# Kernel optimization log

Measured on AMD Instinct MI355X. Metric: run time of the kernel, lower is better.

Reference implementation:

```python
import jax, jax.numpy as jnp
import numpy as np

D_MODEL = 1024
N_HEADS = 16
ADAPTIVE_TEMP = 1.0
LN_EPS = 1e-5


def _sinusoidal_pe(max_len, d_model):
    pos = np.arange(max_len)[:, None].astype(np.float32)
    div = np.exp(np.arange(0, d_model, 2).astype(np.float32) * (-np.log(10000.0) / d_model))
    pe = np.zeros((max_len, d_model), dtype=np.float32)
    pe[:, 0::2] = np.sin(pos * div)
    pe[:, 1::2] = np.cos(pos * div)
    return jnp.asarray(pe)


def _mlp2(q, w1, b1, w2, b2):
    # Linear(1,h) -> ReLU -> Linear(h,d)
    return jax.nn.relu(q @ w1 + b1) @ w2 + b2


def setup_inputs() -> dict:
    key = jax.random.key(0)
    ks = jax.random.split(key, 24)
    B, T, D = 2, 2048, D_MODEL
    H2 = D // 2
    s = 0.02
    inp = {
        "x": jax.random.normal(ks[0], (B, T, D), jnp.float32),
        "quantile": jax.random.uniform(ks[1], (B, 1), jnp.float32),
        "quantile_importance": jax.random.uniform(ks[2], (100,), jnp.float32),
        "Wq": jax.random.normal(ks[3], (D, D), jnp.float32) * s,
        "bq": jnp.zeros((D,), jnp.float32),
        "Wk": jax.random.normal(ks[4], (D, D), jnp.float32) * s,
        "bk": jnp.zeros((D,), jnp.float32),
        "Wv": jax.random.normal(ks[5], (D, D), jnp.float32) * s,
        "bv": jnp.zeros((D,), jnp.float32),
        "Wo": jax.random.normal(ks[6], (D, D), jnp.float32) * s,
        "bo": jnp.zeros((D,), jnp.float32),
        "qpq_w1": jax.random.normal(ks[7], (1, H2), jnp.float32) * s,
        "qpq_b1": jnp.zeros((H2,), jnp.float32),
        "qpq_w2": jax.random.normal(ks[8], (H2, D), jnp.float32) * s,
        "qpq_b2": jnp.zeros((D,), jnp.float32),
        "qpk_w1": jax.random.normal(ks[9], (1, H2), jnp.float32) * s,
        "qpk_b1": jnp.zeros((H2,), jnp.float32),
        "qpk_w2": jax.random.normal(ks[10], (H2, D), jnp.float32) * s,
        "qpk_b2": jnp.zeros((D,), jnp.float32),
        "qpv_w1": jax.random.normal(ks[11], (1, H2), jnp.float32) * s,
        "qpv_b1": jnp.zeros((H2,), jnp.float32),
        "qpv_w2": jax.random.normal(ks[12], (H2, D), jnp.float32) * s,
        "qpv_b2": jnp.zeros((D,), jnp.float32),
        "ln_g": jnp.ones((D,), jnp.float32),
        "ln_b": jnp.zeros((D,), jnp.float32),
    }
    return inp


def reference(x, quantile, quantile_importance,
              Wq, bq, Wk, bk, Wv, bv, Wo, bo,
              qpq_w1, qpq_b1, qpq_w2, qpq_b2,
              qpk_w1, qpk_b1, qpk_w2, qpk_b2,
              qpv_w1, qpv_b1, qpv_w2, qpv_b2,
              ln_g, ln_b):
    B, T, D = x.shape
    H = N_HEADS
    dk = D // H

    # positional encoding
    x = x + _sinusoidal_pe(T, D)

    # quantile-conditioned embeddings [B, D]
    q_embed = _mlp2(quantile, qpq_w1, qpq_b1, qpq_w2, qpq_b2)
    k_embed = _mlp2(quantile, qpk_w1, qpk_b1, qpk_w2, qpk_b2)
    v_embed = _mlp2(quantile, qpv_w1, qpv_b1, qpv_w2, qpv_b2)

    # importance weight per batch (no-grad buffer lookup)
    buf = jax.lax.stop_gradient(quantile_importance)
    idx = jnp.clip((quantile[:, 0] * 100).astype(jnp.int32), 0, 99)
    mx = buf.max()
    imp = buf[idx]
    imp = jnp.where(mx > 0, imp / mx, imp)  # [B]

    Q = (x @ Wq + bq) + q_embed[:, None, :]
    K = (x @ Wk + bk) + k_embed[:, None, :]
    V = (x @ Wv + bv) + v_embed[:, None, :]

    # [B, H, T, dk]
    Q = Q.reshape(B, T, H, dk).transpose(0, 2, 1, 3)
    K = K.reshape(B, T, H, dk).transpose(0, 2, 1, 3)
    V = V.reshape(B, T, H, dk).transpose(0, 2, 1, 3)

    scores = jnp.einsum('bhtd,bhsd->bhts', Q, K) / jnp.sqrt(jnp.float32(dk))
    scale = 1.0 + imp * ADAPTIVE_TEMP  # [B]
    scores = scores * scale[:, None, None, None]

    attn = jax.nn.softmax(scores, axis=-1)  # dropout is identity at inference
    out = jnp.einsum('bhts,bhsd->bhtd', attn, V)
    out = out.transpose(0, 2, 1, 3).reshape(B, T, D)
    out = out @ Wo + bo

    y = x + out
    mu = y.mean(axis=-1, keepdims=True)
    var = y.var(axis=-1, keepdims=True)
    return (y - mu) / jnp.sqrt(var + LN_EPS) * ln_g + ln_b
```

## Files before the change

### kernel.cpp

```cpp
#include <hip/hip_runtime.h>

#define D 1024
#define T 2048
#define BATCH 2
#define NR 4096
#define NH 16
#define HID 512

typedef unsigned short u16;
typedef unsigned int u32;
typedef unsigned long long u64;
typedef float f32x4 __attribute__((ext_vector_type(4)));
typedef float f32x16 __attribute__((ext_vector_type(16)));
typedef __bf16 bf16x8 __attribute__((ext_vector_type(8)));

__device__ __forceinline__ u16 f2bf(float f) {
    union { __bf16 h; u16 u; } c; c.h = (__bf16)f; return c.u;
}

__device__ __forceinline__ u32 cvtpk(float a, float b) {
    u32 r;
    asm("v_cvt_pk_bf16_f32 %0, %1, %2" : "=v"(r) : "v"(a), "v"(b));
    return r;
}

__device__ __forceinline__ void plswap(u32& x, u32& y) {
    asm volatile("v_permlane32_swap_b32 %0, %1" : "+v"(x), "+v"(y));
}

__device__ __forceinline__ float fmax3(float a, float b, float c) {
    float r; asm("v_max3_f32 %0, %1, %2, %3" : "=v"(r) : "v"(a), "v"(b), "v"(c)); return r;
}

__device__ __forceinline__ float vmax16(const f32x16& v) {
    float c0 = fmax3(v[0], v[1], v[2]);
    float c1 = fmax3(v[3], v[4], v[5]);
    float c2 = fmax3(v[6], v[7], v[8]);
    float c3 = fmax3(v[9], v[10], v[11]);
    c0 = fmax3(c0, v[12], v[13]);
    c1 = fmax3(c1, v[14], v[15]);
    c0 = fmax3(c0, c1, c2);
    return fmaxf(c0, c3);
}

__device__ __forceinline__ void gload16(const u16* g, u16* l) {
    __builtin_amdgcn_global_load_lds(
        (const __attribute__((address_space(1))) unsigned int*)g,
        (__attribute__((address_space(3))) unsigned int*)l,
        16, 0, 0);
}

__device__ __forceinline__ int swz8(int row) {
    return (row & 7) ^ ((row >> 3) & 3);
}

__global__ __launch_bounds__(256) void k_mlp1(const float* __restrict__ qtl,
        const float* __restrict__ w1q, const float* __restrict__ b1q, const float* __restrict__ w2q,
        const float* __restrict__ w1k, const float* __restrict__ b1k, const float* __restrict__ w2k,
        const float* __restrict__ w1v, const float* __restrict__ b1v, const float* __restrict__ w2v,
        const float* __restrict__ qimp, float* __restrict__ part, float* __restrict__ scl)
{
    int dc = blockIdx.x;
    int jc = blockIdx.y;
    int wb = blockIdx.z;
    int which = wb >> 1, b = wb & 1;
    const float *w1, *b1, *w2;
    if (which == 0)      { w1 = w1q; b1 = b1q; w2 = w2q; }
    else if (which == 1) { w1 = w1k; b1 = b1k; w2 = w2k; }
    else                 { w1 = w1v; b1 = b1v; w2 = w2v; }
    int tid = threadIdx.x;
    __shared__ float h[128];
    if (tid < 128) {
        int j = jc * 128 + tid;
        h[tid] = fmaxf(qtl[b] * w1[j] + b1[j], 0.0f);
    }
    __syncthreads();
    int d = dc * 256 + tid;
    float acc = 0.0f;
    for (int j = 0; j < 128; ++j) acc += h[j] * w2[(size_t)(jc * 128 + j) * D + d];
    part[((size_t)wb * 4 + jc) * D + d] = acc;
    if (dc == 0 && jc == 0 && wb == 0 && tid < BATCH) {
        float mx = qimp[0];
        for (int i = 1; i < 100; ++i) mx = fmaxf(mx, qimp[i]);
        float q = qtl[tid];
        int idx = (int)(q * 100.0f);
        idx = idx < 0 ? 0 : (idx > 99 ? 99 : idx);
        float imp = qimp[idx];
        if (mx > 0.0f) imp /= mx;
        scl[tid] = 1.0f + imp;
    }
}

__global__ __launch_bounds__(256) void k_mlp2(const float* __restrict__ part,
        const float* __restrict__ b2q, const float* __restrict__ b2k, const float* __restrict__ b2v,
        float* __restrict__ embeds)
{
    int dc = blockIdx.x;
    int wb = blockIdx.y;
    int which = wb >> 1;
    const float* b2 = which == 0 ? b2q : which == 1 ? b2k : b2v;
    int d = dc * 256 + threadIdx.x;
    float acc = b2[d];
    #pragma unroll
    for (int jc = 0; jc < 4; ++jc) acc += part[((size_t)wb * 4 + jc) * D + d];
    embeds[(size_t)wb * D + d] = acc;
}

__global__ __launch_bounds__(256) void k_prep(const float* __restrict__ x,
                                              float* __restrict__ xpe, u16* __restrict__ xpeb,
                                              const float* __restrict__ Wq, const float* __restrict__ Wk,
                                              const float* __restrict__ Wv, const float* __restrict__ Wo,
                                              u16* __restrict__ Wt)
{
    if (blockIdx.x < 4096) {
        int idx = (blockIdx.x * 256 + threadIdx.x) * 4;
        int d = idx & (D - 1);
        int t = (idx >> 10) & (T - 1);
        const float KL = -0.0089944731946f;
        float ft = (float)t;
        float dv0 = __expf((float)d * KL);
        float dv1 = __expf((float)(d + 2) * KL);
        float a0 = ft * dv0, a1 = ft * dv1;
        float4 xv = *reinterpret_cast<const float4*>(x + idx);
        float4 r;
        r.x = xv.x + __sinf(a0);
        r.y = xv.y + __cosf(a0);
        r.z = xv.z + __sinf(a1);
        r.w = xv.w + __cosf(a1);
        *reinterpret_cast<float4*>(xpe + idx) = r;
        ushort4 o;
        o.x = f2bf(r.x); o.y = f2bf(r.y); o.z = f2bf(r.z); o.w = f2bf(r.w);
        *reinterpret_cast<ushort4*>(xpeb + idx) = o;
        return;
    }
    __shared__ float tile[64][65];
    int bi = blockIdx.x - 4096;
    int z = bi >> 8;
    const float* W = z == 0 ? Wq : z == 1 ? Wk : z == 2 ? Wv : Wo;
    u16* out = Wt + (size_t)z * D * D;
    int n0 = (bi & 15) * 64, k0 = ((bi >> 4) & 15) * 64;
    int r = threadIdx.x >> 4;
    int c4 = (threadIdx.x & 15) * 4;
    #pragma unroll
    for (int rr = 0; rr < 64; rr += 16) {
        float4 v = *reinterpret_cast<const float4*>(W + (size_t)(k0 + r + rr) * D + n0 + c4);
        tile[r + rr][c4 + 0] = v.x; tile[r + rr][c4 + 1] = v.y;
        tile[r + rr][c4 + 2] = v.z; tile[r + rr][c4 + 3] = v.w;
    }
    __syncthreads();
    #pragma unroll
    for (int rr = 0; rr < 64; rr += 16) {
        ushort4 o;
        o.x = f2bf(tile[c4 + 0][r + rr]);
        o.y = f2bf(tile[c4 + 1][r + rr]);
        o.z = f2bf(tile[c4 + 2][r + rr]);
        o.w = f2bf(tile[c4 + 3][r + rr]);
        *reinterpret_cast<ushort4*>(out + (size_t)(n0 + r + rr) * D + k0 + c4) = o;
    }
}

__device__ __forceinline__ void gemm128(const u16* __restrict__ Ag, const u16* __restrict__ Bg,
                                        int m0, int n0, f32x16 acc[2][2])
{
    __shared__ u16 As[128 * 64];
    __shared__ u16 Bs[128 * 64];
    const int tid = threadIdx.x;
    const int lane = tid & 63, wave = tid >> 6;
    const int wr = wave >> 1, wc = wave & 1;
    const int l31 = lane & 31, hb = lane >> 5;
    #pragma unroll
    for (int mi = 0; mi < 2; ++mi)
        #pragma unroll
        for (int ni = 0; ni < 2; ++ni)
            #pragma unroll
            for (int e = 0; e < 16; ++e) acc[mi][ni][e] = 0.0f;

    for (int kt = 0; kt < 16; ++kt) {
        __syncthreads();
        #pragma unroll
        for (int c = 0; c < 4; ++c) {
            int ci = c * 256 + tid;
            int row = ci >> 3;
            int sl = (ci & 7) ^ swz8(row);
            gload16(Ag + (size_t)(m0 + row) * D + kt * 64 + sl * 8, As + (size_t)ci * 8);
            gload16(Bg + (size_t)(n0 + row) * D + kt * 64 + sl * 8, Bs + (size_t)ci * 8);
        }
        __syncthreads();
        #pragma unroll
        for (int ks = 0; ks < 4; ++ks) {
            bf16x8 af[2], bfr[2];
            #pragma unroll
            for (int mi = 0; mi < 2; ++mi) {
                int ra = wr * 64 + mi * 32 + l31;
                int sa = (2 * ks + hb) ^ swz8(ra);
                af[mi] = *reinterpret_cast<const bf16x8*>((const char*)As + ra * 128 + sa * 16);
                int rb = wc * 64 + mi * 32 + l31;
                int sb = (2 * ks + hb) ^ swz8(rb);
                bfr[mi] = *reinterpret_cast<const bf16x8*>((const char*)Bs + rb * 128 + sb * 16);
            }
            #pragma unroll
            for (int mi = 0; mi < 2; ++mi)
                #pragma unroll
                for (int ni = 0; ni < 2; ++ni)
                    acc[mi][ni] = __builtin_amdgcn_mfma_f32_32x32x16_bf16(af[mi], bfr[ni], acc[mi][ni], 0, 0, 0);
        }
    }
}

__global__ __launch_bounds__(256, 2)
void k_qkv(const u16* __restrict__ A, const u16* __restrict__ Wt,
           const float* __restrict__ bq, const float* __restrict__ bk, const float* __restrict__ bv,
           const float* __restrict__ embeds, const float* __restrict__ scl,
           u16* __restrict__ Qo, u16* __restrict__ Ko, u16* __restrict__ Vt)
{
    int which = blockIdx.z;
    const u16* Bg = Wt + (size_t)which * D * D;
    const float* bias = which == 0 ? bq : which == 1 ? bk : bv;
    const float* emb = embeds + which * (BATCH * D);
    int m0 = blockIdx.x * 128, n0 = blockIdx.y * 128;
    f32x16 acc[2][2];
    gemm128(A, Bg, m0, n0, acc);
    int lane = threadIdx.x & 63, wave = threadIdx.x >> 6;
    int wr = wave >> 1, wc = wave & 1;
    int l31 = lane & 31, hb = lane >> 5;
    if (which < 2) {
        u16* Out = which == 0 ? Qo : Ko;
        float sc0 = 1.0f, sc1 = 1.0f;
        if (which == 0) {
            sc0 = scl[0] * 0.125f * 1.44269504f;
            sc1 = scl[1] * 0.125f * 1.44269504f;
        }
        #pragma unroll
        for (int ni = 0; ni < 2; ++ni) {
            int c = n0 + wc * 64 + ni * 32 + l31;
            float add0 = bias[c] + emb[c];
            float add1 = bias[c] + emb[D + c];
            #pragma unroll
            for (int mi = 0; mi < 2; ++mi) {
                #pragma unroll
                for (int reg = 0; reg < 16; ++reg) {
                    int r = m0 + wr * 64 + mi * 32 + (reg & 3) + 8 * (reg >> 2) + 4 * hb;
                    float v = (r >> 11) ? (acc[mi][ni][reg] + add1) * sc1
                                        : (acc[mi][ni][reg] + add0) * sc0;
                    Out[(size_t)r * D + c] = f2bf(v);
                }
            }
        }
    } else {
        #pragma unroll
        for (int ni = 0; ni < 2; ++ni) {
            int c = n0 + wc * 64 + ni * 32 + l31;
            int hh = c >> 6, cc = c & 63;
            float add0 = bias[c] + emb[c];
            float add1 = bias[c] + emb[D + c];
            #pragma unroll
            for (int mi = 0; mi < 2; ++mi) {
                #pragma unroll
                for (int g2 = 0; g2 < 4; ++g2) {
                    int r = m0 + wr * 64 + mi * 32 + 8 * g2 + 4 * hb;
                    int bb = r >> 11;
                    int t = r & (T - 1);
                    float add = bb ? add1 : add0;
                    ushort4 o;
                    o.x = f2bf(acc[mi][ni][4 * g2 + 0] + add);
                    o.y = f2bf(acc[mi][ni][4 * g2 + 1] + add);
                    o.z = f2bf(acc[mi][ni][4 * g2 + 2] + add);
                    o.w = f2bf(acc[mi][ni][4 * g2 + 3] + add);
                    *reinterpret_cast<ushort4*>(Vt + ((size_t)((bb * NH + hh) * 64 + cc)) * T + t) = o;
                }
            }
        }
    }
}

__global__ __launch_bounds__(512, 4)
void k_attn(const u16* __restrict__ Q, const u16* __restrict__ K, const u16* __restrict__ Vt,
            u16* __restrict__ AO)
{
    __shared__ u16 Ks[2][2][64 * 64];
    __shared__ u16 Vs[2][2][64 * 64];
    int bh = blockIdx.x;
    int b = bh >> 4, hh = bh & 15;
    int q0 = blockIdx.y * 128;
    int tid = threadIdx.x;
    int lane = tid & 63, w = tid >> 6;
    int half = w >> 2, wq = w & 3;
    int q31 = lane & 31, h = lane >> 5;
    int sh = tid >> 8, sti = tid & 255;
    int kvb = sh * 1024;

    bf16x8 qf[4];
    {
        const u16* qp = Q + (size_t)(b * T + q0 + wq * 32 + q31) * D + hh * 64 + h * 8;
        #pragma unroll
        for (int ds = 0; ds < 4; ++ds)
            qf[ds] = *reinterpret_cast<const bf16x8*>(qp + ds * 16);
    }

    f32x16 o0, o1;
    #pragma unroll
    for (int e = 0; e < 16; ++e) { o0[e] = 0.0f; o1[e] = 0.0f; }
    float m_run = -1e30f, l_run = 0.0f;

    #pragma unroll
    for (int c = 0; c < 2; ++c) {
        int ci = c * 256 + sti;
        int row = ci >> 3;
        int sl = (ci & 7) ^ swz8(row);
        gload16(K + (size_t)(b * T + kvb + row) * D + hh * 64 + sl * 8, Ks[sh][0] + (size_t)ci * 8);
        gload16(Vt + (size_t)(bh * 64 + row) * T + kvb + sl * 8, Vs[sh][0] + (size_t)ci * 8);
    }
    __syncthreads();

    for (int kt = 0; kt < 16; ++kt) {
        int cur = kt & 1;
        if (kt < 15) {
            int t0 = kvb + (kt + 1) * 64;
            #pragma unroll
            for (int c = 0; c < 2; ++c) {
                int ci = c * 256 + sti;
                int row = ci >> 3;
                int sl = (ci & 7) ^ swz8(row);
                gload16(K + (size_t)(b * T + t0 + row) * D + hh * 64 + sl * 8, Ks[sh][cur ^ 1] + (size_t)ci * 8);
                gload16(Vt + (size_t)(bh * 64 + row) * T + t0 + sl * 8, Vs[sh][cur ^ 1] + (size_t)ci * 8);
            }
        }
        const char* Ksc = (const char*)Ks[half][cur];
        const char* Vsc = (const char*)Vs[half][cur];

        f32x16 s[2];
        #pragma unroll
        for (int k2 = 0; k2 < 2; ++k2)
            #pragma unroll
            for (int e = 0; e < 16; ++e) s[k2][e] = 0.0f;
        __builtin_amdgcn_s_setprio(1);
        #pragma unroll
        for (int k2 = 0; k2 < 2; ++k2) {
            int rk = k2 * 32 + q31;
            int xm = swz8(rk);
            #pragma unroll
            for (int ds = 0; ds < 4; ++ds) {
                int sp = (2 * ds + h) ^ xm;
                bf16x8 kf = *reinterpret_cast<const bf16x8*>(Ksc + rk * 128 + sp * 16);
                s[k2] = __builtin_amdgcn_mfma_f32_32x32x16_bf16(kf, qf[ds], s[k2], 0, 0, 0);
            }
        }
        __builtin_amdgcn_s_setprio(0);

        float mt = fmaxf(vmax16(s[0]), vmax16(s[1]));
        mt = fmaxf(mt, __shfl_xor(mt, 32, 64));
        bool skip = __all((int)(mt <= m_run + 11.0f));
        if (!skip) {
            float mn = fmaxf(m_run, mt);
            float corr = __builtin_exp2f(m_run - mn);
            m_run = mn;
            l_run *= corr;
            #pragma unroll
            for (int reg = 0; reg < 16; ++reg) {
                int src = ((reg & 3) + 8 * (reg >> 2)) + ((lane & 32) >> 3);
                float cr = __shfl(corr, src, 64);
                o0[reg] *= cr;
                o1[reg] *= cr;
            }
        }
        float ps0 = 0.0f, ps1 = 0.0f, ps2 = 0.0f, ps3 = 0.0f;
        #pragma unroll
        for (int k2 = 0; k2 < 2; ++k2)
            #pragma unroll
            for (int e = 0; e < 16; ++e) {
                float p = __builtin_exp2f(s[k2][e] - m_run);
                s[k2][e] = p;
                if ((e & 3) == 0) ps0 += p; else if ((e & 3) == 1) ps1 += p;
                else if ((e & 3) == 2) ps2 += p; else ps3 += p;
            }
        float psum = (ps0 + ps1) + (ps2 + ps3);
        psum += __shfl_xor(psum, 32, 64);
        l_run += psum;

        __builtin_amdgcn_s_setprio(1);
        #pragma unroll
        for (int k2 = 0; k2 < 2; ++k2) {
            u32 w0 = cvtpk(s[k2][0], s[k2][1]),   w1 = cvtpk(s[k2][2], s[k2][3]);
            u32 w2 = cvtpk(s[k2][4], s[k2][5]),   w3 = cvtpk(s[k2][6], s[k2][7]);
            u32 w4 = cvtpk(s[k2][8], s[k2][9]),   w5 = cvtpk(s[k2][10], s[k2][11]);
            u32 w6 = cvtpk(s[k2][12], s[k2][13]), w7 = cvtpk(s[k2][14], s[k2][15]);
            plswap(w0, w2); plswap(w1, w3);
            plswap(w4, w6); plswap(w5, w7);
            union { bf16x8 v; u32 u[4]; } plo, phi;
            plo.u[0] = w0; plo.u[1] = w1; plo.u[2] = w2; plo.u[3] = w3;
            phi.u[0] = w4; phi.u[1] = w5; phi.u[2] = w6; phi.u[3] = w7;
            int rv0 = q31, rv1 = 32 + q31;
            int x0 = swz8(rv0), x1 = swz8(rv1);
            int klo = 2 * k2, khi = 2 * k2 + 1;
            bf16x8 vf;
            vf = *reinterpret_cast<const bf16x8*>(Vsc + rv0 * 128 + (((2 * klo + h) ^ x0) << 4));
            o0 = __builtin_amdgcn_mfma_f32_32x32x16_bf16(plo.v, vf, o0, 0, 0, 0);
            vf = *reinterpret_cast<const bf16x8*>(Vsc + rv1 * 128 + (((2 * klo + h) ^ x1) << 4));
            o1 = __builtin_amdgcn_mfma_f32_32x32x16_bf16(plo.v, vf, o1, 0, 0, 0);
            vf = *reinterpret_cast<const bf16x8*>(Vsc + rv0 * 128 + (((2 * khi + h) ^ x0) << 4));
            o0 = __builtin_amdgcn_mfma_f32_32x32x16_bf16(phi.v, vf, o0, 0, 0, 0);
            vf = *reinterpret_cast<const bf16x8*>(Vsc + rv1 * 128 + (((2 * khi + h) ^ x1) << 4));
            o1 = __builtin_amdgcn_mfma_f32_32x32x16_bf16(phi.v, vf, o1, 0, 0, 0);
        }
        __builtin_amdgcn_s_setprio(0);
        __syncthreads();
    }

    float* ML = (float*)Ks;
    float* OB = (float*)Vs;
    if (half == 1) {
        if (h == 0) {
            ML[(wq * 2 + 0) * 32 + q31] = m_run;
            ML[(wq * 2 + 1) * 32 + q31] = l_run;
        }
        #pragma unroll
        for (int reg = 0; reg < 16; ++reg) {
            int row = (reg & 3) + 8 * (reg >> 2) + 4 * h;
            OB[((size_t)wq * 32 + row) * 64 + q31] = o0[reg];
            OB[((size_t)wq * 32 + row) * 64 + 32 + q31] = o1[reg];
        }
    }
    __syncthreads();
    if (half == 0) {
        float mB = ML[(wq * 2 + 0) * 32 + q31];
        float lB = ML[(wq * 2 + 1) * 32 + q31];
        float mn = fmaxf(m_run, mB);
        float ca = __builtin_exp2f(m_run - mn);
        float cb = __builtin_exp2f(mB - mn);
        float lf = ca * l_run + cb * lB;
        float fa = ca / lf, fb = cb / lf;
        #pragma unroll
        for (int reg = 0; reg < 16; ++reg) {
            int src = ((reg & 3) + 8 * (reg >> 2)) + ((lane & 32) >> 3);
            float far = __shfl(fa, src, 64);
            float fbr = __shfl(fb, src, 64);
            int row = (reg & 3) + 8 * (reg >> 2) + 4 * h;
            float b0 = OB[((size_t)wq * 32 + row) * 64 + q31];
            float b1 = OB[((size_t)wq * 32 + row) * 64 + 32 + q31];
            int qr = q0 + wq * 32 + row;
            size_t off = (size_t)(b * T + qr) * D + hh * 64 + q31;
            AO[off] = f2bf(o0[reg] * far + b0 * fbr);
            AO[off + 32] = f2bf(o1[reg] * far + b1 * fbr);
        }
    }
}

__global__ __launch_bounds__(256, 2)
void k_ogemm(const u16* __restrict__ A, const u16* __restrict__ Wt,
             const float* __restrict__ bo, const float* __restrict__ xpe,
             float* __restrict__ y)
{
    int m0 = blockIdx.x * 128, n0 = blockIdx.y * 128;
    f32x16 acc[2][2];
    gemm128(A, Wt, m0, n0, acc);
    int lane = threadIdx.x & 63, wave = threadIdx.x >> 6;
    int wr = wave >> 1, wc = wave & 1;
    int l31 = lane & 31, hb = lane >> 5;
    #pragma unroll
    for (int ni = 0; ni < 2; ++ni) {
        int c = n0 + wc * 64 + ni * 32 + l31;
        float bc = bo[c];
        #pragma unroll
        for (int mi = 0; mi < 2; ++mi) {
            #pragma unroll
            for (int reg = 0; reg < 16; ++reg) {
                int r = m0 + wr * 64 + mi * 32 + (reg & 3) + 8 * (reg >> 2) + 4 * hb;
                y[(size_t)r * D + c] = acc[mi][ni][reg] + bc + xpe[(size_t)r * D + c];
            }
        }
    }
}

__global__ __launch_bounds__(256) void k_ln(const float* __restrict__ y, const float* __restrict__ g,
                                            const float* __restrict__ bb, float* __restrict__ out)
{
    int row = blockIdx.x;
    int tid = threadIdx.x;
    const float* yr = y + (size_t)row * D;
    float4 v = *reinterpret_cast<const float4*>(yr + tid * 4);
    float s = v.x + v.y + v.z + v.w;
    float s2 = v.x * v.x + v.y * v.y + v.z * v.z + v.w * v.w;
    #pragma unroll
    for (int off = 1; off < 64; off <<= 1) {
        s += __shfl_xor(s, off, 64);
        s2 += __shfl_xor(s2, off, 64);
    }
    __shared__ float red[8];
    int wave = tid >> 6, lane = tid & 63;
    if (lane == 0) { red[wave] = s; red[4 + wave] = s2; }
    __syncthreads();
    s = red[0] + red[1] + red[2] + red[3];
    s2 = red[4] + red[5] + red[6] + red[7];
    float mu = s * (1.0f / 1024.0f);
    float var = s2 * (1.0f / 1024.0f) - mu * mu;
    float rstd = rsqrtf(var + 1e-5f);
    float4 gv = *reinterpret_cast<const float4*>(g + tid * 4);
    float4 bv = *reinterpret_cast<const float4*>(bb + tid * 4);
    float4 o;
    o.x = (v.x - mu) * rstd * gv.x + bv.x;
    o.y = (v.y - mu) * rstd * gv.y + bv.y;
    o.z = (v.z - mu) * rstd * gv.z + bv.z;
    o.w = (v.w - mu) * rstd * gv.w + bv.w;
    *reinterpret_cast<float4*>(out + (size_t)row * D + tid * 4) = o;
}

extern "C" void kernel_launch(void* const* d_in, const int* in_sizes, int n_in,
                              void* d_out, int out_size, void* d_ws, size_t ws_size,
                              hipStream_t stream)
{
    const float* x    = (const float*)d_in[0];
    const float* qtl  = (const float*)d_in[1];
    const float* qimp = (const float*)d_in[2];
    const float* Wq = (const float*)d_in[3];
    const float* bq = (const float*)d_in[4];
    const float* Wk = (const float*)d_in[5];
    const float* bk = (const float*)d_in[6];
    const float* Wv = (const float*)d_in[7];
    const float* bv = (const float*)d_in[8];
    const float* Wo = (const float*)d_in[9];
    const float* bo = (const float*)d_in[10];
    const float* qpq_w1 = (const float*)d_in[11];
    const float* qpq_b1 = (const float*)d_in[12];
    const float* qpq_w2 = (const float*)d_in[13];
    const float* qpq_b2 = (const float*)d_in[14];
    const float* qpk_w1 = (const float*)d_in[15];
    const float* qpk_b1 = (const float*)d_in[16];
    const float* qpk_w2 = (const float*)d_in[17];
    const float* qpk_b2 = (const float*)d_in[18];
    const float* qpv_w1 = (const float*)d_in[19];
    const float* qpv_b1 = (const float*)d_in[20];
    const float* qpv_w2 = (const float*)d_in[21];
    const float* qpv_b2 = (const float*)d_in[22];
    const float* ln_g = (const float*)d_in[23];
    const float* ln_b = (const float*)d_in[24];
    (void)in_sizes; (void)n_in; (void)out_size; (void)ws_size;

    char* w = (char*)d_ws;
    float* xpe   = (float*)(w);
    u16* xpeb    = (u16*)(w + (16u << 20));
    u16* Wt      = (u16*)(w + (24u << 20));
    u16* Qb      = (u16*)(w + (32u << 20));
    u16* Kb      = (u16*)(w + (40u << 20));
    u16* Vtb     = (u16*)(w + (48u << 20));
    u16* AOb     = (u16*)(w + (56u << 20));
    float* yb    = (float*)(w + (32u << 20));
    float* emb   = (float*)(w + (64u << 20));
    float* scl   = (float*)(w + (64u << 20) + 32768);
    float* part  = (float*)(w + (64u << 20) + 65536);

    k_mlp1<<<dim3(4, 4, 6), 256, 0, stream>>>(qtl,
        qpq_w1, qpq_b1, qpq_w2,
        qpk_w1, qpk_b1, qpk_w2,
        qpv_w1, qpv_b1, qpv_w2,
        qimp, part, scl);
    k_mlp2<<<dim3(4, 6), 256, 0, stream>>>(part, qpq_b2, qpk_b2, qpv_b2, emb);
    k_prep<<<5120, 256, 0, stream>>>(x, xpe, xpeb, Wq, Wk, Wv, Wo, Wt);
    k_qkv<<<dim3(32, 8, 3), 256, 0, stream>>>(xpeb, Wt, bq, bk, bv, emb, scl, Qb, Kb, Vtb);
    k_attn<<<dim3(32, 16), 512, 0, stream>>>(Qb, Kb, Vtb, AOb);
    k_ogemm<<<dim3(32, 8), 256, 0, stream>>>(AOb, Wt + (size_t)3 * D * D, bo, xpe, yb);
    k_ln<<<4096, 256, 0, stream>>>(yb, ln_g, ln_b, (float*)d_out);
}
```

Measured before the change: 149.0 us.

## Fold MLP embedding kernels into prep and store residual/pre-LN in bf16

Merges the two small quantile-MLP kernels into extra blocks of the prep kernel, removing two launches and the partial-sum buffer. It also drops the fp32 copy of x+PE, with the output GEMM reading the bf16 copy for the residual, and stores the pre-LayerNorm tensor in bf16 rather than fp32. This cuts global memory traffic in prep, ogemm and layernorm at the cost of extra bf16 rounding in the residual and LN input. The 24 MLP blocks now loop over all 512 hidden units serially, which may leave them as a tail on the prep kernel.

Measured after the change: 150.4 us. About the same (+0.9%).

```diff
diff --git a/kernel.cpp b/kernel.cpp
--- a/kernel.cpp
+++ b/kernel.cpp
@@ -16,6 +16,9 @@
 
 __device__ __forceinline__ u16 f2bf(float f) {
     union { __bf16 h; u16 u; } c; c.h = (__bf16)f; return c.u;
+}
+__device__ __forceinline__ float bf2f(u16 u) {
+    union { u32 u; float f; } c; c.u = ((u32)u) << 16; return c.f;
 }
 
 __device__ __forceinline__ u32 cvtpk(float a, float b) {
@@ -54,32 +57,78 @@
     return (row & 7) ^ ((row >> 3) & 3);
 }
 
-__global__ __launch_bounds__(256) void k_mlp1(const float* __restrict__ qtl,
-        const float* __restrict__ w1q, const float* __restrict__ b1q, const float* __restrict__ w2q,
-        const float* __restrict__ w1k, const float* __restrict__ b1k, const float* __restrict__ w2k,
-        const float* __restrict__ w1v, const float* __restrict__ b1v, const float* __restrict__ w2v,
-        const float* __restrict__ qimp, float* __restrict__ part, float* __restrict__ scl)
-{
-    int dc = blockIdx.x;
-    int jc = blockIdx.y;
-    int wb = blockIdx.z;
+__global__ __launch_bounds__(256) void k_prep(const float* __restrict__ x, u16* __restrict__ xpeb,
+        const float* __restrict__ Wq, const float* __restrict__ Wk,
+        const float* __restrict__ Wv, const float* __restrict__ Wo, u16* __restrict__ Wt,
+        const float* __restrict__ qtl, const float* __restrict__ qimp,
+        const float* __restrict__ w1q, const float* __restrict__ b1q, const float* __restrict__ w2q, const float* __restrict__ b2q,
+        const float* __restrict__ w1k, const float* __restrict__ b1k, const float* __restrict__ w2k, const float* __restrict__ b2k,
+        const float* __restrict__ w1v, const float* __restrict__ b1v, const float* __restrict__ w2v, const float* __restrict__ b2v,
+        float* __restrict__ embeds, float* __restrict__ scl)
+{
+    int tid = threadIdx.x;
+    if (blockIdx.x < 4096) {
+        int idx = (blockIdx.x * 256 + tid) * 4;
+        int d = idx & (D - 1);
+        int t = (idx >> 10) & (T - 1);
+        const float KL = -0.0089944731946f;
+        float ft = (float)t;
+        float dv0 = __expf((float)d * KL);
+        float dv1 = __expf((float)(d + 2) * KL);
+        float a0 = ft * dv0, a1 = ft * dv1;
+        float4 xv = *reinterpret_cast<const float4*>(x + idx);
+        ushort4 o;
+        o.x = f2bf(xv.x + __sinf(a0));
+        o.y = f2bf(xv.y + __cosf(a0));
+        o.z = f2bf(xv.z + __sinf(a1));
+        o.w = f2bf(xv.w + __cosf(a1));
+        *reinterpret_cast<ushort4*>(xpeb + idx) = o;
+        return;
+    }
+    if (blockIdx.x < 5120) {
+        __shared__ float tile[64][65];
+        int bi = blockIdx.x - 4096;
+        int z = bi >> 8;
+        const float* W = z == 0 ? Wq : z == 1 ? Wk : z == 2 ? Wv : Wo;
+        u16* out = Wt + (size_t)z * D * D;
+        int n0 = (bi & 15) * 64, k0 = ((bi >> 4) & 15) * 64;
+        int r = tid >> 4;
+        int c4 = (tid & 15) * 4;
+        #pragma unroll
+        for (int rr = 0; rr < 64; rr += 16) {
+            float4 v = *reinterpret_cast<const float4*>(W + (size_t)(k0 + r + rr) * D + n0 + c4);
+            tile[r + rr][c4 + 0] = v.x; tile[r + rr][c4 + 1] = v.y;
+            tile[r + rr][c4 + 2] = v.z; tile[r + rr][c4 + 3] = v.w;
+        }
+        __syncthreads();
+        #pragma unroll
+        for (int rr = 0; rr < 64; rr += 16) {
+            ushort4 o;
+            o.x = f2bf(tile[c4 + 0][r + rr]);
+            o.y = f2bf(tile[c4 + 1][r + rr]);
+            o.z = f2bf(tile[c4 + 2][r + rr]);
+            o.w = f2bf(tile[c4 + 3][r + rr]);
+            *reinterpret_cast<ushort4*>(out + (size_t)(n0 + r + rr) * D + k0 + c4) = o;
+        }
+        return;
+    }
+    __shared__ float h[HID];
+    int bi2 = blockIdx.x - 5120;
+    int dc = bi2 & 3, wb = bi2 >> 2;
     int which = wb >> 1, b = wb & 1;
-    const float *w1, *b1, *w2;
-    if (which == 0)      { w1 = w1q; b1 = b1q; w2 = w2q; }
-    else if (which == 1) { w1 = w1k; b1 = b1k; w2 = w2k; }
-    else                 { w1 = w1v; b1 = b1v; w2 = w2v; }
-    int tid = threadIdx.x;
-    __shared__ float h[128];
-    if (tid < 128) {
-        int j = jc * 128 + tid;
-        h[tid] = fmaxf(qtl[b] * w1[j] + b1[j], 0.0f);
-    }
+    const float *w1, *b1, *w2, *b2;
+    if (which == 0)      { w1 = w1q; b1 = b1q; w2 = w2q; b2 = b2q; }
+    else if (which == 1) { w1 = w1k; b1 = b1k; w2 = w2k; b2 = b2k; }
+    else                 { w1 = w1v; b1 = b1v; w2 = w2v; b2 = b2v; }
+    float qv = qtl[b];
+    h[tid] = fmaxf(qv * w1[tid] + b1[tid], 0.0f);
+    h[tid + 256] = fmaxf(qv * w1[tid + 256] + b1[tid + 256], 0.0f);
     __syncthreads();
     int d = dc * 256 + tid;
-    float acc = 0.0f;
-    for (int j = 0; j < 128; ++j) acc += h[j] * w2[(size_t)(jc * 128 + j) * D + d];
-    part[((size_t)wb * 4 + jc) * D + d] = acc;
-    if (dc == 0 && jc == 0 && wb == 0 && tid < BATCH) {
+    float acc = b2[d];
+    for (int j = 0; j < HID; ++j) acc += h[j] * w2[(size_t)j * D + d];
+    embeds[(size_t)wb * D + d] = acc;
+    if (bi2 == 0 && tid < BATCH) {
         float mx = qimp[0];
         for (int i = 1; i < 100; ++i) mx = fmaxf(mx, qimp[i]);
         float q = qtl[tid];
@@ -88,74 +137,6 @@
         float imp = qimp[idx];
         if (mx > 0.0f) imp /= mx;
         scl[tid] = 1.0f + imp;
-    }
-}
-
-__global__ __launch_bounds__(256) void k_mlp2(const float* __restrict__ part,
-        const float* __restrict__ b2q, const float* __restrict__ b2k, const float* __restrict__ b2v,
-        float* __restrict__ embeds)
-{
-    int dc = blockIdx.x;
-    int wb = blockIdx.y;
-    int which = wb >> 1;
-    const float* b2 = which == 0 ? b2q : which == 1 ? b2k : b2v;
-    int d = dc * 256 + threadIdx.x;
-    float acc = b2[d];
-    #pragma unroll
-    for (int jc = 0; jc < 4; ++jc) acc += part[((size_t)wb * 4 + jc) * D + d];
-    embeds[(size_t)wb * D + d] = acc;
-}
-
-__global__ __launch_bounds__(256) void k_prep(const float* __restrict__ x,
-                                              float* __restrict__ xpe, u16* __restrict__ xpeb,
-                                              const float* __restrict__ Wq, const float* __restrict__ Wk,
-                                              const float* __restrict__ Wv, const float* __restrict__ Wo,
-                                              u16* __restrict__ Wt)
-{
-    if (blockIdx.x < 4096) {
-        int idx = (blockIdx.x * 256 + threadIdx.x) * 4;
-        int d = idx & (D - 1);
-        int t = (idx >> 10) & (T - 1);
-        const float KL = -0.0089944731946f;
-        float ft = (float)t;
-        float dv0 = __expf((float)d * KL);
-        float dv1 = __expf((float)(d + 2) * KL);
-        float a0 = ft * dv0, a1 = ft * dv1;
-        float4 xv = *reinterpret_cast<const float4*>(x + idx);
-        float4 r;
-        r.x = xv.x + __sinf(a0);
-        r.y = xv.y + __cosf(a0);
-        r.z = xv.z + __sinf(a1);
-        r.w = xv.w + __cosf(a1);
-        *reinterpret_cast<float4*>(xpe + idx) = r;
-        ushort4 o;
-        o.x = f2bf(r.x); o.y = f2bf(r.y); o.z = f2bf(r.z); o.w = f2bf(r.w);
-        *reinterpret_cast<ushort4*>(xpeb + idx) = o;
-        return;
-    }
-    __shared__ float tile[64][65];
-    int bi = blockIdx.x - 4096;
-    int z = bi >> 8;
-    const float* W = z == 0 ? Wq : z == 1 ? Wk : z == 2 ? Wv : Wo;
-    u16* out = Wt + (size_t)z * D * D;
-    int n0 = (bi & 15) * 64, k0 = ((bi >> 4) & 15) * 64;
-    int r = threadIdx.x >> 4;
-    int c4 = (threadIdx.x & 15) * 4;
-    #pragma unroll
-    for (int rr = 0; rr < 64; rr += 16) {
-        float4 v = *reinterpret_cast<const float4*>(W + (size_t)(k0 + r + rr) * D + n0 + c4);
-        tile[r + rr][c4 + 0] = v.x; tile[r + rr][c4 + 1] = v.y;
-        tile[r + rr][c4 + 2] = v.z; tile[r + rr][c4 + 3] = v.w;
-    }
-    __syncthreads();
-    #pragma unroll
-    for (int rr = 0; rr < 64; rr += 16) {
-        ushort4 o;
-        o.x = f2bf(tile[c4 + 0][r + rr]);
-        o.y = f2bf(tile[c4 + 1][r + rr]);
-        o.z = f2bf(tile[c4 + 2][r + rr]);
-        o.w = f2bf(tile[c4 + 3][r + rr]);
-        *reinterpret_cast<ushort4*>(out + (size_t)(n0 + r + rr) * D + k0 + c4) = o;
     }
 }
 
@@ -447,8 +428,8 @@
 
 __global__ __launch_bounds__(256, 2)
 void k_ogemm(const u16* __restrict__ A, const u16* __restrict__ Wt,
-             const float* __restrict__ bo, const float* __restrict__ xpe,
-             float* __restrict__ y)
+             const float* __restrict__ bo, const u16* __restrict__ xpeb,
+             u16* __restrict__ y)
 {
     int m0 = blockIdx.x * 128, n0 = blockIdx.y * 128;
     f32x16 acc[2][2];
@@ -465,21 +446,23 @@
             #pragma unroll
             for (int reg = 0; reg < 16; ++reg) {
                 int r = m0 + wr * 64 + mi * 32 + (reg & 3) + 8 * (reg >> 2) + 4 * hb;
-                y[(size_t)r * D + c] = acc[mi][ni][reg] + bc + xpe[(size_t)r * D + c];
-            }
-        }
-    }
-}
-
-__global__ __launch_bounds__(256) void k_ln(const float* __restrict__ y, const float* __restrict__ g,
+                float res = bf2f(xpeb[(size_t)r * D + c]);
+                y[(size_t)r * D + c] = f2bf(acc[mi][ni][reg] + bc + res);
+            }
+        }
+    }
+}
+
+__global__ __launch_bounds__(256) void k_ln(const u16* __restrict__ y, const float* __restrict__ g,
                                             const float* __restrict__ bb, float* __restrict__ out)
 {
     int row = blockIdx.x;
     int tid = threadIdx.x;
-    const float* yr = y + (size_t)row * D;
-    float4 v = *reinterpret_cast<const float4*>(yr + tid * 4);
-    float s = v.x + v.y + v.z + v.w;
-    float s2 = v.x * v.x + v.y * v.y + v.z * v.z + v.w * v.w;
+    const u16* yr = y + (size_t)row * D;
+    ushort4 v4 = *reinterpret_cast<const ushort4*>(yr + tid * 4);
+    float v0 = bf2f(v4.x), v1 = bf2f(v4.y), v2 = bf2f(v4.z), v3 = bf2f(v4.w);
+    float s = (v0 + v1) + (v2 + v3);
+    float s2 = (v0 * v0 + v1 * v1) + (v2 * v2 + v3 * v3);
     #pragma unroll
     for (int off = 1; off < 64; off <<= 1) {
         s += __shfl_xor(s, off, 64);
@@ -497,10 +480,10 @@
     float4 gv = *reinterpret_cast<const float4*>(g + tid * 4);
     float4 bv = *reinterpret_cast<const float4*>(bb + tid * 4);
     float4 o;
-    o.x = (v.x - mu) * rstd * gv.x + bv.x;
-    o.y = (v.y - mu) * rstd * gv.y + bv.y;
-    o.z = (v.z - mu) * rstd * gv.z + bv.z;
-    o.w = (v.w - mu) * rstd * gv.w + bv.w;
+    o.x = (v0 - mu) * rstd * gv.x + bv.x;
+    o.y = (v1 - mu) * rstd * gv.y + bv.y;
+    o.z = (v2 - mu) * rstd * gv.z + bv.z;
+    o.w = (v3 - mu) * rstd * gv.w + bv.w;
     *reinterpret_cast<float4*>(out + (size_t)row * D + tid * 4) = o;
 }
 
@@ -536,27 +519,24 @@
     (void)in_sizes; (void)n_in; (void)out_size; (void)ws_size;
 
     char* w = (char*)d_ws;
-    float* xpe   = (float*)(w);
-    u16* xpeb    = (u16*)(w + (16u << 20));
-    u16* Wt      = (u16*)(w + (24u << 20));
-    u16* Qb      = (u16*)(w + (32u << 20));
-    u16* Kb      = (u16*)(w + (40u << 20));
-    u16* Vtb     = (u16*)(w + (48u << 20));
-    u16* AOb     = (u16*)(w + (56u << 20));
-    float* yb    = (float*)(w + (32u << 20));
-    float* emb   = (float*)(w + (64u << 20));
-    float* scl   = (float*)(w + (64u << 20) + 32768);
-    float* part  = (float*)(w + (64u << 20) + 65536);
-
-    k_mlp1<<<dim3(4, 4, 6), 256, 0, stream>>>(qtl,
-        qpq_w1, qpq_b1, qpq_w2,
-        qpk_w1, qpk_b1, qpk_w2,
-        qpv_w1, qpv_b1, qpv_w2,
-        qimp, part, scl);
-    k_mlp2<<<dim3(4, 6), 256, 0, stream>>>(part, qpq_b2, qpk_b2, qpv_b2, emb);
-    k_prep<<<5120, 256, 0, stream>>>(x, xpe, xpeb, Wq, Wk, Wv, Wo, Wt);
+    u16* xpeb    = (u16*)(w);
+    u16* Wt      = (u16*)(w + (8u << 20));
+    u16* Qb      = (u16*)(w + (16u << 20));
+    u16* Kb      = (u16*)(w + (24u << 20));
+    u16* Vtb     = (u16*)(w + (32u << 20));
+    u16* AOb     = (u16*)(w + (40u << 20));
+    u16* yb      = (u16*)(w + (16u << 20));
+    float* emb   = (float*)(w + (48u << 20));
+    float* scl   = (float*)(w + (48u << 20) + 32768);
+
+    k_prep<<<5144, 256, 0, stream>>>(x, xpeb, Wq, Wk, Wv, Wo, Wt,
+        qtl, qimp,
+        qpq_w1, qpq_b1, qpq_w2, qpq_b2,
+        qpk_w1, qpk_b1, qpk_w2, qpk_b2,
+        qpv_w1, qpv_b1, qpv_w2, qpv_b2,
+        emb, scl);
     k_qkv<<<dim3(32, 8, 3), 256, 0, stream>>>(xpeb, Wt, bq, bk, bv, emb, scl, Qb, Kb, Vtb);
     k_attn<<<dim3(32, 16), 512, 0, stream>>>(Qb, Kb, Vtb, AOb);
-    k_ogemm<<<dim3(32, 8), 256, 0, stream>>>(AOb, Wt + (size_t)3 * D * D, bo, xpe, yb);
+    k_ogemm<<<dim3(32, 8), 256, 0, stream>>>(AOb, Wt + (size_t)3 * D * D, bo, xpeb, yb);
     k_ln<<<4096, 256, 0, stream>>>(yb, ln_g, ln_b, (float*)d_out);
 }
```
